# Kernel tuning notes

Hardware: AMD Instinct MI355X
Metric: run time of the kernel (lower is better)

Reference implementation:

```python
import jax, jax.numpy as jnp
import numpy as np

N, E, D, ATT = 20000, 5000, 128, 32
NUM_LAYERS = 4
LN_EPS = 1e-5
DEG_EPS = 1e-12

def setup_inputs() -> dict:
    key = jax.random.key(0)
    k1, k2, k3, k4 = jax.random.split(key, 4)
    node_embeddings = jax.random.normal(k1, (N, D), dtype=jnp.float32)
    hypergraph_matrix = (jax.random.uniform(k2, (N, E)) < 0.01).astype(jnp.float32)
    ln_gamma = jnp.ones((D,), jnp.float32)
    ln_beta = jnp.zeros((D,), jnp.float32)
    W_att = jax.random.normal(k3, (D, ATT), dtype=jnp.float32) * (1.0 / np.sqrt(D))
    b_att = jnp.zeros((ATT,), jnp.float32)
    q_att = jax.random.normal(k4, (ATT,), dtype=jnp.float32)
    return {"node_embeddings": node_embeddings, "hypergraph_matrix": hypergraph_matrix,
            "ln_gamma": ln_gamma, "ln_beta": ln_beta,
            "W_att": W_att, "b_att": b_att, "q_att": q_att}

def _layernorm(y, gamma, beta):
    mu = jnp.mean(y, axis=-1, keepdims=True)
    var = jnp.mean(jnp.square(y - mu), axis=-1, keepdims=True)
    return (y - mu) * jax.lax.rsqrt(var + LN_EPS) * gamma + beta

def reference(node_embeddings, hypergraph_matrix, ln_gamma, ln_beta, W_att, b_att, q_att):
    H = hypergraph_matrix                      # [N, E]
    dv_inv = 1.0 / jnp.maximum(jnp.sum(H, axis=1), DEG_EPS)   # [N]
    de_inv = 1.0 / jnp.maximum(jnp.sum(H, axis=0), DEG_EPS)   # [E]
    x = node_embeddings
    for _ in range(NUM_LAYERS):
        edge_mean = (H.T @ x) * de_inv[:, None]       # V->E mean, [E, D]
        node_msg = (H @ edge_mean) * dv_inv[:, None]  # E->V mean, [N, D]
        x = _layernorm(node_msg + node_embeddings, ln_gamma, ln_beta)
        # dropout(p=0.35) is identity in eval mode
    # per-edge masked mean over member nodes (vectorized segment-mean)
    M = (H > 0).astype(x.dtype)                        # [N, E]
    cnt = jnp.maximum(jnp.sum(M, axis=0), 1.0)         # [E]
    edge_out = (M.T @ x) / cnt[:, None]                # [E, D]
    # dot-product attention pooling over hyperedges
    scores = jax.nn.softmax(jnp.tanh(edge_out @ W_att + b_att) @ q_att)  # [E]
    return scores @ edge_out                           # [D]
```

## Files before the change

kernel.cpp:

```cpp
#include <hip/hip_runtime.h>
#include <hip/hip_fp16.h>
#include <math.h>

#define NN 20000
#define EE 5000
#define DD 128
#define ATT 32
#define NUM_LAYERS 4
#define LN_EPS 1e-5f
#define DEG_EPS 1e-12f

#define ECAP 320
#define NCAP 128
#define CSTRIDE 32

typedef float vfloat4 __attribute__((ext_vector_type(4)));

__device__ inline unsigned pack2h(float x, float y) {
    return __builtin_bit_cast(unsigned, __floats2half2_rn(x, y));
}
__device__ inline void acc8(float* a, uint4 u) {
    __half2 h;
    h = __builtin_bit_cast(__half2, u.x); a[0] += __low2float(h); a[1] += __high2float(h);
    h = __builtin_bit_cast(__half2, u.y); a[2] += __low2float(h); a[3] += __high2float(h);
    h = __builtin_bit_cast(__half2, u.z); a[4] += __low2float(h); a[5] += __high2float(h);
    h = __builtin_bit_cast(__half2, u.w); a[6] += __low2float(h); a[7] += __high2float(h);
}


__global__ __launch_bounds__(256) void build_adj(
    const float* __restrict__ H, int* __restrict__ cur, int* __restrict__ nc,
    int* __restrict__ el, int* __restrict__ nl,
    const float* __restrict__ x0, __half* __restrict__ xh0) {
    const int n = blockIdx.x;
    const int tid = threadIdx.x;
    __shared__ int lcnt;
    __shared__ int lbuf[NCAP];
    if (tid == 0) lcnt = 0;
    __syncthreads();
    const vfloat4* row = reinterpret_cast<const vfloat4*>(H + (size_t)n * EE);
    for (int i = tid; i < EE / 4; i += 256) {
        const vfloat4 h = __builtin_nontemporal_load(row + i);
        float v[4] = {h.x, h.y, h.z, h.w};
        const int ebase = i * 4;
#pragma unroll
        for (int k = 0; k < 4; k++) {
            if (v[k] != 0.0f) {
                int s = atomicAdd(&lcnt, 1);
                if (s < NCAP) lbuf[s] = ebase + k;
            }
        }
    }
    __syncthreads();
    const int c = min(lcnt, NCAP);
    for (int k = tid; k < c; k += 256) {
        const int e = lbuf[k];
        nl[(size_t)n * NCAP + k] = e;
        const int slot = atomicAdd(&cur[e << 5], 1);
        if (slot < ECAP) el[(size_t)e * ECAP + slot] = n;
    }
    if (tid < 64) {
        const float2 v = reinterpret_cast<const float2*>(x0 + (size_t)n * DD)[tid];
        reinterpret_cast<unsigned*>(xh0 + (size_t)n * DD)[tid] = pack2h(v.x, v.y);
    }
    if (tid == 0) nc[n] = lcnt;
}

template <bool FINAL>
__global__ __launch_bounds__(256) void edge_gather16(
    const __half* __restrict__ xh, const int* __restrict__ cur,
    const int* __restrict__ el, __half* __restrict__ outh,
    float* __restrict__ eout, const float* __restrict__ W,
    const float* __restrict__ bb, const float* __restrict__ qv,
    float* __restrict__ t) {
    __shared__ int ilst[ECAP];
    __shared__ float part[4][16][8];
    __shared__ float rowbuf[DD];
    const int e = blockIdx.x;
    const int tid = threadIdx.x;
    const int* lst = el + (size_t)e * ECAP;
    ilst[tid] = lst[tid];
    if (tid < ECAP - 256) ilst[256 + tid] = lst[256 + tid];
    const int cnt = cur[e << 5];
    const int c = min(cnt, ECAP);
    __syncthreads();
    const int lane16 = tid & 15;
    const int s = tid >> 4;
    const int wave = tid >> 6;
    float a[8] = {0, 0, 0, 0, 0, 0, 0, 0};
    float b[8] = {0, 0, 0, 0, 0, 0, 0, 0};
    int i = s;
    for (; i + 112 < c; i += 128) {
        const int n0 = ilst[i];
        const int n1 = ilst[i + 16];
        const int n2 = ilst[i + 32];
        const int n3 = ilst[i + 48];
        const int n4 = ilst[i + 64];
        const int n5 = ilst[i + 80];
        const int n6 = ilst[i + 96];
        const int n7 = ilst[i + 112];
        const uint4 u0 = *reinterpret_cast<const uint4*>(xh + n0 * DD + lane16 * 8);
        const uint4 u1 = *reinterpret_cast<const uint4*>(xh + n1 * DD + lane16 * 8);
        const uint4 u2 = *reinterpret_cast<const uint4*>(xh + n2 * DD + lane16 * 8);
        const uint4 u3 = *reinterpret_cast<const uint4*>(xh + n3 * DD + lane16 * 8);
        const uint4 u4 = *reinterpret_cast<const uint4*>(xh + n4 * DD + lane16 * 8);
        const uint4 u5 = *reinterpret_cast<const uint4*>(xh + n5 * DD + lane16 * 8);
        const uint4 u6 = *reinterpret_cast<const uint4*>(xh + n6 * DD + lane16 * 8);
        const uint4 u7 = *reinterpret_cast<const uint4*>(xh + n7 * DD + lane16 * 8);
        acc8(a, u0); acc8(b, u1); acc8(a, u2); acc8(b, u3);
        acc8(a, u4); acc8(b, u5); acc8(a, u6); acc8(b, u7);
    }
    for (; i + 48 < c; i += 64) {
        const int n0 = ilst[i];
        const int n1 = ilst[i + 16];
        const int n2 = ilst[i + 32];
        const int n3 = ilst[i + 48];
        const uint4 u0 = *reinterpret_cast<const uint4*>(xh + n0 * DD + lane16 * 8);
        const uint4 u1 = *reinterpret_cast<const uint4*>(xh + n1 * DD + lane16 * 8);
        const uint4 u2 = *reinterpret_cast<const uint4*>(xh + n2 * DD + lane16 * 8);
        const uint4 u3 = *reinterpret_cast<const uint4*>(xh + n3 * DD + lane16 * 8);
        acc8(a, u0); acc8(b, u1); acc8(a, u2); acc8(b, u3);
    }
    for (; i + 16 < c; i += 32) {
        const int n0 = ilst[i];
        const int n1 = ilst[i + 16];
        const uint4 u0 = *reinterpret_cast<const uint4*>(xh + n0 * DD + lane16 * 8);
        const uint4 u1 = *reinterpret_cast<const uint4*>(xh + n1 * DD + lane16 * 8);
        acc8(a, u0); acc8(b, u1);
    }
    if (i < c) {
        acc8(a, *reinterpret_cast<const uint4*>(xh + ilst[i] * DD + lane16 * 8));
    }
#pragma unroll
    for (int k = 0; k < 8; k++) {
        float v = a[k] + b[k];
        v += __shfl_down(v, 16);
        v += __shfl_down(v, 32);
        a[k] = v;
    }
    if ((tid & 63) < 16) {
#pragma unroll
        for (int k = 0; k < 8; k++) part[wave][lane16][k] = a[k];
    }
    __syncthreads();
    if (tid < 16) {
        const float inv = 1.0f / fmaxf((float)cnt, DEG_EPS);
        float o[8];
#pragma unroll
        for (int k = 0; k < 8; k++)
            o[k] = (part[0][tid][k] + part[1][tid][k] + part[2][tid][k] + part[3][tid][k]) * inv;
        if (!FINAL) {
            uint4 u;
            u.x = pack2h(o[0], o[1]); u.y = pack2h(o[2], o[3]);
            u.z = pack2h(o[4], o[5]); u.w = pack2h(o[6], o[7]);
            *reinterpret_cast<uint4*>(outh + e * DD + tid * 8) = u;
        } else {
#pragma unroll
            for (int k = 0; k < 8; k++) rowbuf[tid * 8 + k] = o[k];
            *reinterpret_cast<float4*>(eout + e * DD + tid * 8) =
                make_float4(o[0], o[1], o[2], o[3]);
            *reinterpret_cast<float4*>(eout + e * DD + tid * 8 + 4) =
                make_float4(o[4], o[5], o[6], o[7]);
        }
    }
    if (FINAL) {
        __syncthreads();
        float r = 0.0f;
        if (tid < ATT) {
            float acc = 0.0f;
#pragma unroll 4
            for (int d = 0; d < DD; d++) acc += rowbuf[d] * W[d * ATT + tid];
            r = tanhf(acc + bb[tid]) * qv[tid];
        }
        for (int off = 16; off > 0; off >>= 1) r += __shfl_down(r, off);
        if (tid == 0) t[e] = r;
    }
}

__global__ __launch_bounds__(128) void node_gather_ln16(
    const __half* __restrict__ emean, const int* __restrict__ nc,
    const int* __restrict__ nl, const float* __restrict__ x0,
    const float* __restrict__ gamma, const float* __restrict__ beta,
    __half* __restrict__ xout) {
    __shared__ int ilst[NCAP];
    __shared__ float part[2][16][8];
    const int n = blockIdx.x;
    const int tid = threadIdx.x;
    const int* lst = nl + (size_t)n * NCAP;
    ilst[tid] = lst[tid];
    const int cnt = nc[n];
    const int c = min(cnt, NCAP);
    __syncthreads();
    const int lane16 = tid & 15;
    const int s = tid >> 4;
    const int wave = tid >> 6;
    float a[8] = {0, 0, 0, 0, 0, 0, 0, 0};
    float b[8] = {0, 0, 0, 0, 0, 0, 0, 0};
    int i = s;
    for (; i + 24 < c; i += 32) {
        const int e0 = ilst[i];
        const int e1 = ilst[i + 8];
        const int e2 = ilst[i + 16];
        const int e3 = ilst[i + 24];
        const uint4 u0 = *reinterpret_cast<const uint4*>(emean + e0 * DD + lane16 * 8);
        const uint4 u1 = *reinterpret_cast<const uint4*>(emean + e1 * DD + lane16 * 8);
        const uint4 u2 = *reinterpret_cast<const uint4*>(emean + e2 * DD + lane16 * 8);
        const uint4 u3 = *reinterpret_cast<const uint4*>(emean + e3 * DD + lane16 * 8);
        acc8(a, u0); acc8(b, u1); acc8(a, u2); acc8(b, u3);
    }
    for (; i + 8 < c; i += 16) {
        const int e0 = ilst[i];
        const int e1 = ilst[i + 8];
        const uint4 u0 = *reinterpret_cast<const uint4*>(emean + e0 * DD + lane16 * 8);
        const uint4 u1 = *reinterpret_cast<const uint4*>(emean + e1 * DD + lane16 * 8);
        acc8(a, u0); acc8(b, u1);
    }
    if (i < c) {
        acc8(a, *reinterpret_cast<const uint4*>(emean + ilst[i] * DD + lane16 * 8));
    }
#pragma unroll
    for (int k = 0; k < 8; k++) {
        float v = a[k] + b[k];
        v += __shfl_down(v, 16);
        v += __shfl_down(v, 32);
        a[k] = v;
    }
    if ((tid & 63) < 16) {
#pragma unroll
        for (int k = 0; k < 8; k++) part[wave][lane16][k] = a[k];
    }
    __syncthreads();
    if (tid < 16) {
        const float inv = 1.0f / fmaxf((float)cnt, DEG_EPS);
        const float4 x0a = *reinterpret_cast<const float4*>(x0 + n * DD + tid * 8);
        const float4 x0b = *reinterpret_cast<const float4*>(x0 + n * DD + tid * 8 + 4);
        float y[8];
        y[0] = (part[0][tid][0] + part[1][tid][0]) * inv + x0a.x;
        y[1] = (part[0][tid][1] + part[1][tid][1]) * inv + x0a.y;
        y[2] = (part[0][tid][2] + part[1][tid][2]) * inv + x0a.z;
        y[3] = (part[0][tid][3] + part[1][tid][3]) * inv + x0a.w;
        y[4] = (part[0][tid][4] + part[1][tid][4]) * inv + x0b.x;
        y[5] = (part[0][tid][5] + part[1][tid][5]) * inv + x0b.y;
        y[6] = (part[0][tid][6] + part[1][tid][6]) * inv + x0b.z;
        y[7] = (part[0][tid][7] + part[1][tid][7]) * inv + x0b.w;
        float sm = 0.0f, ss = 0.0f;
#pragma unroll
        for (int k = 0; k < 8; k++) { sm += y[k]; ss += y[k] * y[k]; }
        for (int off = 8; off > 0; off >>= 1) {
            sm += __shfl_down(sm, off);
            ss += __shfl_down(ss, off);
        }
        sm = __shfl(sm, 0);
        ss = __shfl(ss, 0);
        const float mu = sm * (1.0f / 128.0f);
        float var = ss * (1.0f / 128.0f) - mu * mu;
        var = fmaxf(var, 0.0f);
        const float rstd = 1.0f / sqrtf(var + LN_EPS);
        const float4 g0 = *reinterpret_cast<const float4*>(gamma + tid * 8);
        const float4 g1 = *reinterpret_cast<const float4*>(gamma + tid * 8 + 4);
        const float4 b0 = *reinterpret_cast<const float4*>(beta + tid * 8);
        const float4 b1 = *reinterpret_cast<const float4*>(beta + tid * 8 + 4);
        float gg[8] = {g0.x, g0.y, g0.z, g0.w, g1.x, g1.y, g1.z, g1.w};
        float bb[8] = {b0.x, b0.y, b0.z, b0.w, b1.x, b1.y, b1.z, b1.w};
        float o[8];
#pragma unroll
        for (int k = 0; k < 8; k++) o[k] = (y[k] - mu) * rstd * gg[k] + bb[k];
        uint4 u;
        u.x = pack2h(o[0], o[1]); u.y = pack2h(o[2], o[3]);
        u.z = pack2h(o[4], o[5]); u.w = pack2h(o[6], o[7]);
        *reinterpret_cast<uint4*>(xout + n * DD + tid * 8) = u;
    }
}

__global__ __launch_bounds__(1024) void softmax_stats(
    const float* __restrict__ t, float* __restrict__ MS) {
    __shared__ float red[16];
    __shared__ float smax;
    const int tid = threadIdx.x;
    const int wid = tid >> 6;
    float m = -1e30f;
    for (int i = tid; i < EE; i += 1024) m = fmaxf(m, t[i]);
    for (int off = 32; off > 0; off >>= 1) m = fmaxf(m, __shfl_down(m, off));
    if ((tid & 63) == 0) red[wid] = m;
    __syncthreads();
    if (tid < 64) {
        float v = (tid < 16) ? red[tid] : -1e30f;
        for (int off = 8; off > 0; off >>= 1) v = fmaxf(v, __shfl_down(v, off));
        if (tid == 0) smax = v;
    }
    __syncthreads();
    const float M = smax;
    float sum = 0.0f;
    for (int i = tid; i < EE; i += 1024) sum += expf(t[i] - M);
    for (int off = 32; off > 0; off >>= 1) sum += __shfl_down(sum, off);
    if ((tid & 63) == 0) red[wid] = sum;
    __syncthreads();
    if (tid < 64) {
        float v = (tid < 16) ? red[tid] : 0.0f;
        for (int off = 8; off > 0; off >>= 1) v += __shfl_down(v, off);
        if (tid == 0) { MS[0] = M; MS[1] = v; }
    }
}

__global__ __launch_bounds__(128) void weighted_sum(
    const float* __restrict__ eout, const float* __restrict__ t,
    const float* __restrict__ MS, float* __restrict__ out) {
    const int d = threadIdx.x;
    const float M = MS[0];
    const float invS = 1.0f / MS[1];
    float acc = 0.0f;
    for (int e = blockIdx.x; e < EE; e += gridDim.x) {
        const float w = expf(t[e] - M);
        acc += w * eout[e * DD + d];
    }
    atomicAdd(&out[d], acc * invS);
}

extern "C" void kernel_launch(void* const* d_in, const int* in_sizes, int n_in,
                              void* d_out, int out_size, void* d_ws, size_t ws_size,
                              hipStream_t stream) {
    const float* x0 = (const float*)d_in[0];
    const float* H = (const float*)d_in[1];
    const float* gamma = (const float*)d_in[2];
    const float* beta = (const float*)d_in[3];
    const float* W = (const float*)d_in[4];
    const float* b = (const float*)d_in[5];
    const float* qv = (const float*)d_in[6];
    float* out = (float*)d_out;

    char* w = (char*)d_ws;
    int* cur = (int*)w;       w += (size_t)EE * CSTRIDE * 4;
    int* nc = (int*)w;        w += (size_t)NN * 4;
    int* el = (int*)w;        w += (size_t)EE * ECAP * 4;
    int* nl = (int*)w;        w += (size_t)NN * NCAP * 4;
    __half* xh = (__half*)w;  w += (size_t)NN * DD * 2;
    __half* emean = (__half*)w; w += (size_t)EE * DD * 2;
    float* eout = (float*)w;  w += (size_t)EE * DD * 4;
    float* t = (float*)w;     w += (size_t)EE * 4;
    float* MS = (float*)w;    w += 16;

    hipMemsetAsync(cur, 0, (size_t)EE * CSTRIDE * 4, stream);
    hipMemsetAsync(d_out, 0, (size_t)DD * sizeof(float), stream);

    build_adj<<<NN, 256, 0, stream>>>(H, cur, nc, el, nl, x0, xh);

    for (int l = 0; l < NUM_LAYERS; l++) {
        edge_gather16<false><<<EE, 256, 0, stream>>>(
            xh, cur, el, emean, nullptr, nullptr, nullptr, nullptr, nullptr);
        node_gather_ln16<<<NN, 128, 0, stream>>>(
            emean, nc, nl, x0, gamma, beta, xh);
    }

    edge_gather16<true><<<EE, 256, 0, stream>>>(
        xh, cur, el, nullptr, eout, W, b, qv, t);
    softmax_stats<<<1, 1024, 0, stream>>>(t, MS);
    weighted_sum<<<256, 128, 0, stream>>>(eout, t, MS, out);
}
```

Measured before the change: 740.5 us.

## Replace sparse gather propagation with dense fp16 MFMA GEMMs over incidence matrix

```diff
diff --git a/kernel.cpp b/kernel.cpp
--- a/kernel.cpp
+++ b/kernel.cpp
@@ -15,6 +15,11 @@
 #define CSTRIDE 32
 
 typedef float vfloat4 __attribute__((ext_vector_type(4)));
+typedef _Float16 f16;
+typedef f16 f16x8 __attribute__((ext_vector_type(8)));
+typedef float f32x4 __attribute__((ext_vector_type(4)));
+typedef unsigned short ushort_t;
+typedef unsigned int uint_t;
 
 __device__ inline unsigned pack2h(float x, float y) {
     return __builtin_bit_cast(unsigned, __floats2half2_rn(x, y));
@@ -27,6 +32,316 @@
     h = __builtin_bit_cast(__half2, u.w); a[6] += __low2float(h); a[7] += __high2float(h);
 }
 
+
+#define LP 36
+
+__device__ inline f16x8 ld8(const ushort_t* p) {
+    uint2 a = *(const uint2*)p;
+    uint2 b = *(const uint2*)(p + 4);
+    union { uint_t u[4]; f16x8 v; } x;
+    x.u[0] = a.x; x.u[1] = a.y; x.u[2] = b.x; x.u[3] = b.y;
+    return x.v;
+}
+
+__global__ __launch_bounds__(256) void convert_h(
+    const float* __restrict__ H, __half* __restrict__ H16,
+    int* __restrict__ cur, int* __restrict__ nc,
+    const float* __restrict__ x0, __half* __restrict__ xh) {
+    const int n = blockIdx.x;
+    const int t = threadIdx.x;
+    __shared__ int red[4];
+    int cnt = 0;
+    const vfloat4* row = reinterpret_cast<const vfloat4*>(H + (size_t)n * EE);
+    uint2* orow = reinterpret_cast<uint2*>(H16 + (size_t)n * EE);
+    for (int i = t; i < EE / 4; i += 256) {
+        const vfloat4 h = __builtin_nontemporal_load(row + i);
+        uint2 u; u.x = pack2h(h.x, h.y); u.y = pack2h(h.z, h.w);
+        orow[i] = u;
+        const int e = i * 4;
+        if (h.x != 0.0f) { cnt++; atomicAdd(&cur[(e + 0) << 5], 1); }
+        if (h.y != 0.0f) { cnt++; atomicAdd(&cur[(e + 1) << 5], 1); }
+        if (h.z != 0.0f) { cnt++; atomicAdd(&cur[(e + 2) << 5], 1); }
+        if (h.w != 0.0f) { cnt++; atomicAdd(&cur[(e + 3) << 5], 1); }
+    }
+    for (int off = 32; off > 0; off >>= 1) cnt += __shfl_down(cnt, off);
+    if ((t & 63) == 0) red[t >> 6] = cnt;
+    if (t < 64) {
+        const float2 v = reinterpret_cast<const float2*>(x0 + (size_t)n * DD)[t];
+        reinterpret_cast<unsigned*>(xh + (size_t)n * DD)[t] = pack2h(v.x, v.y);
+    }
+    __syncthreads();
+    if (t == 0) nc[n] = red[0] + red[1] + red[2] + red[3];
+}
+
+__global__ __launch_bounds__(256) void gemm_e(
+    const __half* __restrict__ H16, const __half* __restrict__ xh,
+    float* __restrict__ Cacc) {
+    __shared__ ushort_t Asm[64][LP];
+    __shared__ ushort_t Bsm[128][LP];
+    const int bid = blockIdx.x;
+    const int mt_ = bid % 79, kc = bid / 79;
+    const int e0 = mt_ * 64;
+    const int kbeg = kc * 5000, kend = kbeg + 5000;
+    const int t = threadIdx.x;
+    const int w = t >> 6, l = t & 63;
+    const int lr = l & 15, lk = l >> 4;
+    f32x4 acc[4][2];
+#pragma unroll
+    for (int m = 0; m < 4; m++)
+#pragma unroll
+        for (int nt = 0; nt < 2; nt++) acc[m][nt] = (f32x4){0.f, 0.f, 0.f, 0.f};
+    const int B_kp = t >> 4, B_dg = t & 15;
+    const int A_kp = (t & 127) >> 3, A_eg = t & 7;
+    const ushort_t* H16u = (const ushort_t*)H16;
+    const ushort_t* xhu = (const ushort_t*)xh;
+    for (int k0 = kbeg; k0 < kend; k0 += 32) {
+        uint4 r0 = {0,0,0,0}, r1 = {0,0,0,0}, s0 = {0,0,0,0}, s1 = {0,0,0,0};
+        {
+            const int ka = k0 + 2 * B_kp, kb = ka + 1;
+            if (ka < kend) r0 = *(const uint4*)(xhu + (size_t)ka * DD + B_dg * 8);
+            if (kb < kend) r1 = *(const uint4*)(xhu + (size_t)kb * DD + B_dg * 8);
+        }
+        if (t < 128) {
+            const int ka = k0 + 2 * A_kp, kb = ka + 1;
+            if (ka < kend) s0 = *(const uint4*)(H16u + (size_t)ka * EE + e0 + A_eg * 8);
+            if (kb < kend) s1 = *(const uint4*)(H16u + (size_t)kb * EE + e0 + A_eg * 8);
+        }
+        __syncthreads();
+        {
+            const ushort_t* p0 = (const ushort_t*)&r0;
+            const ushort_t* p1 = (const ushort_t*)&r1;
+#pragma unroll
+            for (int i = 0; i < 8; i++) {
+                *(uint_t*)&Bsm[B_dg * 8 + i][2 * B_kp] =
+                    (uint_t)p0[i] | ((uint_t)p1[i] << 16);
+            }
+            if (t < 128) {
+                const ushort_t* q0 = (const ushort_t*)&s0;
+                const ushort_t* q1 = (const ushort_t*)&s1;
+#pragma unroll
+                for (int i = 0; i < 8; i++) {
+                    *(uint_t*)&Asm[A_eg * 8 + i][2 * A_kp] =
+                        (uint_t)q0[i] | ((uint_t)q1[i] << 16);
+                }
+            }
+        }
+        __syncthreads();
+        f16x8 bfrag[2], afrag[4];
+#pragma unroll
+        for (int nt = 0; nt < 2; nt++)
+            bfrag[nt] = ld8(&Bsm[w * 32 + nt * 16 + lr][lk * 8]);
+#pragma unroll
+        for (int m = 0; m < 4; m++)
+            afrag[m] = ld8(&Asm[m * 16 + lr][lk * 8]);
+#pragma unroll
+        for (int m = 0; m < 4; m++)
+#pragma unroll
+            for (int nt = 0; nt < 2; nt++)
+                acc[m][nt] = __builtin_amdgcn_mfma_f32_16x16x32_f16(
+                    afrag[m], bfrag[nt], acc[m][nt], 0, 0, 0);
+    }
+#pragma unroll
+    for (int m = 0; m < 4; m++)
+#pragma unroll
+        for (int nt = 0; nt < 2; nt++)
+#pragma unroll
+            for (int r = 0; r < 4; r++) {
+                const int e = e0 + m * 16 + lk * 4 + r;
+                const int d = w * 32 + nt * 16 + lr;
+                atomicAdd(&Cacc[(size_t)e * DD + d], acc[m][nt][r]);
+            }
+}
+
+__global__ __launch_bounds__(256) void ep_edge(
+    float* __restrict__ Cacc, const int* __restrict__ cur,
+    __half* __restrict__ em, float* __restrict__ eout, const int isFinal) {
+    const int e = blockIdx.x * 2 + (threadIdx.x >> 7);
+    const int d = threadIdx.x & 127;
+    const float v = Cacc[(size_t)e * DD + d];
+    Cacc[(size_t)e * DD + d] = 0.0f;
+    if (e >= EE) return;
+    const float de = (float)cur[e << 5];
+    if (!isFinal) {
+        const float s = 1.0f / fmaxf(de, DEG_EPS);
+        em[(size_t)e * DD + d] = (__half)(v * s);
+    } else {
+        const float s = 1.0f / fmaxf(de, 1.0f);
+        eout[(size_t)e * DD + d] = v * s;
+    }
+}
+
+__global__ __launch_bounds__(256) void gemm_n(
+    const __half* __restrict__ H16, const __half* __restrict__ em,
+    const int* __restrict__ nc, const float* __restrict__ x0,
+    const float* __restrict__ gamma, const float* __restrict__ beta,
+    __half* __restrict__ xh) {
+    __shared__ ushort_t Asm[64][LP];
+    __shared__ ushort_t Bsm[128][LP];
+    __shared__ float Csm[64][DD];
+    const int n0 = blockIdx.x * 64;
+    const int t = threadIdx.x;
+    const int w = t >> 6, l = t & 63;
+    const int lr = l & 15, lk = l >> 4;
+    f32x4 acc[4][2];
+#pragma unroll
+    for (int m = 0; m < 4; m++)
+#pragma unroll
+        for (int nt = 0; nt < 2; nt++) acc[m][nt] = (f32x4){0.f, 0.f, 0.f, 0.f};
+    const int A_m = t >> 2, A_kg = t & 3;
+    const int B_kp = t >> 4, B_dg = t & 15;
+    const ushort_t* H16u = (const ushort_t*)H16;
+    const ushort_t* emu = (const ushort_t*)em;
+    for (int k0 = 0; k0 < EE; k0 += 32) {
+        uint4 r0 = {0,0,0,0}, r1 = {0,0,0,0}, s0 = {0,0,0,0};
+        {
+            const int ka = k0 + 2 * B_kp, kb = ka + 1;
+            if (ka < EE) r0 = *(const uint4*)(emu + (size_t)ka * DD + B_dg * 8);
+            if (kb < EE) r1 = *(const uint4*)(emu + (size_t)kb * DD + B_dg * 8);
+        }
+        if (n0 + A_m < NN && k0 + A_kg * 8 < EE)
+            s0 = *(const uint4*)(H16u + (size_t)(n0 + A_m) * EE + k0 + A_kg * 8);
+        __syncthreads();
+        {
+            const ushort_t* p0 = (const ushort_t*)&r0;
+            const ushort_t* p1 = (const ushort_t*)&r1;
+#pragma unroll
+            for (int i = 0; i < 8; i++) {
+                *(uint_t*)&Bsm[B_dg * 8 + i][2 * B_kp] =
+                    (uint_t)p0[i] | ((uint_t)p1[i] << 16);
+            }
+            uint2* adst = (uint2*)&Asm[A_m][A_kg * 8];
+            adst[0] = make_uint2(s0.x, s0.y);
+            adst[1] = make_uint2(s0.z, s0.w);
+        }
+        __syncthreads();
+        f16x8 bfrag[2], afrag[4];
+#pragma unroll
+        for (int nt = 0; nt < 2; nt++)
+            bfrag[nt] = ld8(&Bsm[w * 32 + nt * 16 + lr][lk * 8]);
+#pragma unroll
+        for (int m = 0; m < 4; m++)
+            afrag[m] = ld8(&Asm[m * 16 + lr][lk * 8]);
+#pragma unroll
+        for (int m = 0; m < 4; m++)
+#pragma unroll
+            for (int nt = 0; nt < 2; nt++)
+                acc[m][nt] = __builtin_amdgcn_mfma_f32_16x16x32_f16(
+                    afrag[m], bfrag[nt], acc[m][nt], 0, 0, 0);
+    }
+#pragma unroll
+    for (int m = 0; m < 4; m++)
+#pragma unroll
+        for (int nt = 0; nt < 2; nt++)
+#pragma unroll
+            for (int r = 0; r < 4; r++)
+                Csm[m * 16 + lk * 4 + r][w * 32 + nt * 16 + lr] = acc[m][nt][r];
+    __syncthreads();
+    const int nn = t >> 2, q = t & 3;
+    const int n = n0 + nn;
+    if (n < NN) {
+        const float dvinv = 1.0f / fmaxf((float)nc[n], DEG_EPS);
+        float y[32];
+        float sm = 0.0f, ss = 0.0f;
+#pragma unroll
+        for (int j = 0; j < 8; j++) {
+            const float4 c = *(const float4*)&Csm[nn][q * 32 + j * 4];
+            const float4 xr = *(const float4*)(x0 + (size_t)n * DD + q * 32 + j * 4);
+            float v0 = c.x * dvinv + xr.x, v1 = c.y * dvinv + xr.y;
+            float v2 = c.z * dvinv + xr.z, v3 = c.w * dvinv + xr.w;
+            y[j * 4 + 0] = v0; y[j * 4 + 1] = v1; y[j * 4 + 2] = v2; y[j * 4 + 3] = v3;
+            sm += v0 + v1 + v2 + v3;
+            ss += v0 * v0 + v1 * v1 + v2 * v2 + v3 * v3;
+        }
+        sm += __shfl_xor(sm, 1); sm += __shfl_xor(sm, 2);
+        ss += __shfl_xor(ss, 1); ss += __shfl_xor(ss, 2);
+        const float mu = sm * (1.0f / 128.0f);
+        float var = ss * (1.0f / 128.0f) - mu * mu;
+        var = fmaxf(var, 0.0f);
+        const float rstd = 1.0f / sqrtf(var + LN_EPS);
+        uint_t ou[16];
+#pragma unroll
+        for (int j = 0; j < 8; j++) {
+            const float4 g = *(const float4*)(gamma + q * 32 + j * 4);
+            const float4 bb = *(const float4*)(beta + q * 32 + j * 4);
+            const float o0 = (y[j * 4 + 0] - mu) * rstd * g.x + bb.x;
+            const float o1 = (y[j * 4 + 1] - mu) * rstd * g.y + bb.y;
+            const float o2 = (y[j * 4 + 2] - mu) * rstd * g.z + bb.z;
+            const float o3 = (y[j * 4 + 3] - mu) * rstd * g.w + bb.w;
+            ou[j * 2 + 0] = pack2h(o0, o1);
+            ou[j * 2 + 1] = pack2h(o2, o3);
+        }
+        uint4* dst = (uint4*)(xh + (size_t)n * DD + q * 32);
+#pragma unroll
+        for (int j = 0; j < 4; j++)
+            dst[j] = make_uint4(ou[j * 4], ou[j * 4 + 1], ou[j * 4 + 2], ou[j * 4 + 3]);
+    }
+}
+
+__global__ __launch_bounds__(64) void logits(
+    const float* __restrict__ eout, const float* __restrict__ W,
+    const float* __restrict__ bb, const float* __restrict__ qv,
+    float* __restrict__ t) {
+    __shared__ float rowbuf[DD];
+    const int e = blockIdx.x;
+    const int tid = threadIdx.x;
+    const float2 v = reinterpret_cast<const float2*>(eout + (size_t)e * DD)[tid];
+    rowbuf[tid * 2] = v.x;
+    rowbuf[tid * 2 + 1] = v.y;
+    __syncthreads();
+    float r = 0.0f;
+    if (tid < ATT) {
+        float acc = 0.0f;
+#pragma unroll 4
+        for (int d = 0; d < DD; d++) acc += rowbuf[d] * W[d * ATT + tid];
+        r = tanhf(acc + bb[tid]) * qv[tid];
+    }
+    for (int off = 16; off > 0; off >>= 1) r += __shfl_down(r, off);
+    if (tid == 0) t[e] = r;
+}
+
+__global__ __launch_bounds__(1024) void softmax_stats(
+    const float* __restrict__ t, float* __restrict__ MS) {
+    __shared__ float red[16];
+    __shared__ float smax;
+    const int tid = threadIdx.x;
+    const int wid = tid >> 6;
+    float m = -1e30f;
+    for (int i = tid; i < EE; i += 1024) m = fmaxf(m, t[i]);
+    for (int off = 32; off > 0; off >>= 1) m = fmaxf(m, __shfl_down(m, off));
+    if ((tid & 63) == 0) red[wid] = m;
+    __syncthreads();
+    if (tid < 64) {
+        float v = (tid < 16) ? red[tid] : -1e30f;
+        for (int off = 8; off > 0; off >>= 1) v = fmaxf(v, __shfl_down(v, off));
+        if (tid == 0) smax = v;
+    }
+    __syncthreads();
+    const float M = smax;
+    float sum = 0.0f;
+    for (int i = tid; i < EE; i += 1024) sum += expf(t[i] - M);
+    for (int off = 32; off > 0; off >>= 1) sum += __shfl_down(sum, off);
+    if ((tid & 63) == 0) red[wid] = sum;
+    __syncthreads();
+    if (tid < 64) {
+        float v = (tid < 16) ? red[tid] : 0.0f;
+        for (int off = 8; off > 0; off >>= 1) v += __shfl_down(v, off);
+        if (tid == 0) { MS[0] = M; MS[1] = v; }
+    }
+}
+
+__global__ __launch_bounds__(128) void weighted_sum(
+    const float* __restrict__ eout, const float* __restrict__ t,
+    const float* __restrict__ MS, float* __restrict__ out) {
+    const int d = threadIdx.x;
+    const float M = MS[0];
+    const float invS = 1.0f / MS[1];
+    float acc = 0.0f;
+    for (int e = blockIdx.x; e < EE; e += gridDim.x) {
+        const float w = expf(t[e] - M);
+        acc += w * eout[e * DD + d];
+    }
+    atomicAdd(&out[d], acc * invS);
+}
 
 __global__ __launch_bounds__(256) void build_adj(
     const float* __restrict__ H, int* __restrict__ cur, int* __restrict__ nc,
@@ -90,26 +405,6 @@
     float a[8] = {0, 0, 0, 0, 0, 0, 0, 0};
     float b[8] = {0, 0, 0, 0, 0, 0, 0, 0};
     int i = s;
-    for (; i + 112 < c; i += 128) {
-        const int n0 = ilst[i];
-        const int n1 = ilst[i + 16];
-        const int n2 = ilst[i + 32];
-        const int n3 = ilst[i + 48];
-        const int n4 = ilst[i + 64];
-        const int n5 = ilst[i + 80];
-        const int n6 = ilst[i + 96];
-        const int n7 = ilst[i + 112];
-        const uint4 u0 = *reinterpret_cast<const uint4*>(xh + n0 * DD + lane16 * 8);
-        const uint4 u1 = *reinterpret_cast<const uint4*>(xh + n1 * DD + lane16 * 8);
-        const uint4 u2 = *reinterpret_cast<const uint4*>(xh + n2 * DD + lane16 * 8);
-        const uint4 u3 = *reinterpret_cast<const uint4*>(xh + n3 * DD + lane16 * 8);
-        const uint4 u4 = *reinterpret_cast<const uint4*>(xh + n4 * DD + lane16 * 8);
-        const uint4 u5 = *reinterpret_cast<const uint4*>(xh + n5 * DD + lane16 * 8);
-        const uint4 u6 = *reinterpret_cast<const uint4*>(xh + n6 * DD + lane16 * 8);
-        const uint4 u7 = *reinterpret_cast<const uint4*>(xh + n7 * DD + lane16 * 8);
-        acc8(a, u0); acc8(b, u1); acc8(a, u2); acc8(b, u3);
-        acc8(a, u4); acc8(b, u5); acc8(a, u6); acc8(b, u7);
-    }
     for (; i + 48 < c; i += 64) {
         const int n0 = ilst[i];
         const int n1 = ilst[i + 16];
@@ -272,50 +567,6 @@
     }
 }
 
-__global__ __launch_bounds__(1024) void softmax_stats(
-    const float* __restrict__ t, float* __restrict__ MS) {
-    __shared__ float red[16];
-    __shared__ float smax;
-    const int tid = threadIdx.x;
-    const int wid = tid >> 6;
-    float m = -1e30f;
-    for (int i = tid; i < EE; i += 1024) m = fmaxf(m, t[i]);
-    for (int off = 32; off > 0; off >>= 1) m = fmaxf(m, __shfl_down(m, off));
-    if ((tid & 63) == 0) red[wid] = m;
-    __syncthreads();
-    if (tid < 64) {
-        float v = (tid < 16) ? red[tid] : -1e30f;
-        for (int off = 8; off > 0; off >>= 1) v = fmaxf(v, __shfl_down(v, off));
-        if (tid == 0) smax = v;
-    }
-    __syncthreads();
-    const float M = smax;
-    float sum = 0.0f;
-    for (int i = tid; i < EE; i += 1024) sum += expf(t[i] - M);
-    for (int off = 32; off > 0; off >>= 1) sum += __shfl_down(sum, off);
-    if ((tid & 63) == 0) red[wid] = sum;
-    __syncthreads();
-    if (tid < 64) {
-        float v = (tid < 16) ? red[tid] : 0.0f;
-        for (int off = 8; off > 0; off >>= 1) v += __shfl_down(v, off);
-        if (tid == 0) { MS[0] = M; MS[1] = v; }
-    }
-}
-
-__global__ __launch_bounds__(128) void weighted_sum(
-    const float* __restrict__ eout, const float* __restrict__ t,
-    const float* __restrict__ MS, float* __restrict__ out) {
-    const int d = threadIdx.x;
-    const float M = MS[0];
-    const float invS = 1.0f / MS[1];
-    float acc = 0.0f;
-    for (int e = blockIdx.x; e < EE; e += gridDim.x) {
-        const float w = expf(t[e] - M);
-        acc += w * eout[e * DD + d];
-    }
-    atomicAdd(&out[d], acc * invS);
-}
-
 extern "C" void kernel_launch(void* const* d_in, const int* in_sizes, int n_in,
                               void* d_out, int out_size, void* d_ws, size_t ws_size,
                               hipStream_t stream) {
@@ -328,31 +579,53 @@
     const float* qv = (const float*)d_in[6];
     float* out = (float*)d_out;
 
-    char* w = (char*)d_ws;
-    int* cur = (int*)w;       w += (size_t)EE * CSTRIDE * 4;
-    int* nc = (int*)w;        w += (size_t)NN * 4;
-    int* el = (int*)w;        w += (size_t)EE * ECAP * 4;
-    int* nl = (int*)w;        w += (size_t)NN * NCAP * 4;
-    __half* xh = (__half*)w;  w += (size_t)NN * DD * 2;
-    __half* emean = (__half*)w; w += (size_t)EE * DD * 2;
-    float* eout = (float*)w;  w += (size_t)EE * DD * 4;
-    float* t = (float*)w;     w += (size_t)EE * 4;
-    float* MS = (float*)w;    w += 16;
+    size_t off = 0;
+    auto alloc = [&](size_t bytes) -> char* {
+        char* p = (char*)d_ws + off;
+        off += (bytes + 255) & ~(size_t)255;
+        return p;
+    };
+    int* cur = (int*)alloc((size_t)EE * CSTRIDE * 4);
+    int* nc = (int*)alloc((size_t)NN * 4);
+    int* el = (int*)alloc((size_t)EE * ECAP * 4);
+    int* nl = (int*)alloc((size_t)NN * NCAP * 4);
+    __half* xh = (__half*)alloc((size_t)NN * DD * 2);
+    __half* emean = (__half*)alloc((size_t)EE * DD * 2);
+    float* eout = (float*)alloc((size_t)EE * DD * 4);
+    float* t = (float*)alloc((size_t)EE * 4);
+    float* MS = (float*)alloc(64);
+    float* Cacc = (float*)alloc((size_t)5056 * DD * 4);
+    const size_t h16_bytes = (size_t)NN * EE * 2;
+    __half* H16 = (__half*)alloc(h16_bytes);
+    const bool use_gemm = (off <= ws_size);
 
     hipMemsetAsync(cur, 0, (size_t)EE * CSTRIDE * 4, stream);
     hipMemsetAsync(d_out, 0, (size_t)DD * sizeof(float), stream);
 
-    build_adj<<<NN, 256, 0, stream>>>(H, cur, nc, el, nl, x0, xh);
-
-    for (int l = 0; l < NUM_LAYERS; l++) {
-        edge_gather16<false><<<EE, 256, 0, stream>>>(
-            xh, cur, el, emean, nullptr, nullptr, nullptr, nullptr, nullptr);
-        node_gather_ln16<<<NN, 128, 0, stream>>>(
-            emean, nc, nl, x0, gamma, beta, xh);
-    }
-
-    edge_gather16<true><<<EE, 256, 0, stream>>>(
-        xh, cur, el, nullptr, eout, W, b, qv, t);
-    softmax_stats<<<1, 1024, 0, stream>>>(t, MS);
-    weighted_sum<<<256, 128, 0, stream>>>(eout, t, MS, out);
-}
+    if (use_gemm) {
+        hipMemsetAsync(Cacc, 0, (size_t)5056 * DD * 4, stream);
+        convert_h<<<NN, 256, 0, stream>>>(H, H16, cur, nc, x0, xh);
+        for (int l = 0; l < NUM_LAYERS; l++) {
+            gemm_e<<<79 * 4, 256, 0, stream>>>(H16, xh, Cacc);
+            ep_edge<<<2528, 256, 0, stream>>>(Cacc, cur, emean, nullptr, 0);
+            gemm_n<<<313, 256, 0, stream>>>(H16, emean, nc, x0, gamma, beta, xh);
+        }
+        gemm_e<<<79 * 4, 256, 0, stream>>>(H16, xh, Cacc);
+        ep_edge<<<2528, 256, 0, stream>>>(Cacc, cur, nullptr, eout, 1);
+        logits<<<EE, 64, 0, stream>>>(eout, W, b, qv, t);
+        softmax_stats<<<1, 1024, 0, stream>>>(t, MS);
+        weighted_sum<<<256, 128, 0, stream>>>(eout, t, MS, out);
+    } else {
+        build_adj<<<NN, 256, 0, stream>>>(H, cur, nc, el, nl, x0, xh);
+        for (int l = 0; l < NUM_LAYERS; l++) {
+            edge_gather16<false><<<EE, 256, 0, stream>>>(
+                xh, cur, el, emean, nullptr, nullptr, nullptr, nullptr, nullptr);
+            node_gather_ln16<<<NN, 128, 0, stream>>>(
+                emean, nc, nl, x0, gamma, beta, xh);
+        }
+        edge_gather16<true><<<EE, 256, 0, stream>>>(
+            xh, cur, el, nullptr, eout, W, b, qv, t);
+        softmax_stats<<<1, 1024, 0, stream>>>(t, MS);
+        weighted_sum<<<256, 128, 0, stream>>>(eout, t, MS, out);
+    }
+}
```

Measured after the change: 2.671 ms. +260.6%, slower.
